# Optimization experiments

Hardware: AMD Instinct MI355X
Metric: run time of the kernel (lower is better)

## Reference

```python
import jax, jax.numpy as jnp
import numpy as np
import math

H = 128      # hidden_channels
R = 32       # num_rbf
N = 4096     # atoms
E = 65536    # edges
CU = 4.5     # cutoff_upper (cutoff_lower = 0)
ALPHA = 5.0 / CU
MEANS = jnp.linspace(math.exp(-CU), 1.0, R, dtype=jnp.float32)
BETA = jnp.float32((2.0 / R * (1.0 - math.exp(-CU))) ** -2)
EPS = 1e-5


def _ln(x, g, b):
    mu = x.mean(-1, keepdims=True)
    var = ((x - mu) ** 2).mean(-1, keepdims=True)
    return (x - mu) * jax.lax.rsqrt(var + EPS) * g + b


def setup_inputs() -> dict:
    key = jax.random.key(0)
    ks = jax.random.split(key, 20)
    f32 = jnp.float32

    def w(i, shape):
        return jax.random.normal(ks[i], shape, f32) / np.float32(np.sqrt(shape[-1]))

    return {
        "edge_vec": jax.random.normal(ks[0], (E, 3), f32) * 1.5,
        "emb_w": w(1, (128, H)),
        "emb2_w": w(2, (H, 2 * H)), "emb2_b": jnp.zeros((H,), f32),
        "dp1_w": w(3, (H, R)), "dp1_b": jnp.zeros((H,), f32),
        "dp2_w": w(4, (H, R)), "dp2_b": jnp.zeros((H,), f32),
        "dp3_w": w(5, (H, R)), "dp3_b": jnp.zeros((H,), f32),
        "lt0_w": w(6, (H, H)), "lt1_w": w(7, (H, H)), "lt2_w": w(8, (H, H)),
        "ls0_w": w(9, (2 * H, H)), "ls0_b": jnp.zeros((2 * H,), f32),
        "ls1_w": w(10, (3 * H, 2 * H)), "ls1_b": jnp.zeros((3 * H,), f32),
        "init_g": jnp.ones((H,), f32), "init_b": jnp.zeros((H,), f32),
        "lin_w": w(11, (H, 3 * H)), "lin_b": jnp.zeros((H,), f32),
        "outn_g": jnp.ones((3 * H,), f32), "outn_b": jnp.zeros((3 * H,), f32),
        "ol1_w": w(12, (H // 2, H)), "ol1_b": jnp.zeros((H // 2,), f32),
        "ol2_w": w(13, (1, H // 2)), "ol2_b": jnp.zeros((1,), f32),
        "z": jax.random.randint(ks[14], (N,), 0, 128, dtype=jnp.int32),
        "edge_index": jax.random.randint(ks[15], (2, E), 0, N, dtype=jnp.int32),
    }


def reference(edge_vec, emb_w, emb2_w, emb2_b, dp1_w, dp1_b, dp2_w, dp2_b,
              dp3_w, dp3_b, lt0_w, lt1_w, lt2_w, ls0_w, ls0_b, ls1_w, ls1_b,
              init_g, init_b, lin_w, lin_b, outn_g, outn_b, ol1_w, ol1_b,
              ol2_w, ol2_b, z, edge_index):
    n = z.shape[0]
    src, dst = edge_index[0], edge_index[1]

    d = jnp.sqrt((edge_vec ** 2).sum(-1))                 # (E,)
    vn = edge_vec / d[:, None]                             # unit edge vectors
    cut = jnp.where(d < CU, 0.5 * (jnp.cos(jnp.pi * d / CU) + 1.0), 0.0)
    # expnorm RBF
    rbf = cut[:, None] * jnp.exp(-BETA * (jnp.exp(-ALPHA * d)[:, None] - MEANS) ** 2)  # (E,R)

    # atomic-number message Zij = emb2(cat(emb(z_i), emb(z_j)))
    zpair = jnp.concatenate([emb_w[z[src]], emb_w[z[dst]]], -1)  # (E,2H)
    zij = zpair @ emb2_w.T + emb2_b                              # (E,H)
    c = cut[:, None] * zij                                       # cutoff * Zij, (E,H)

    w1 = (rbf @ dp1_w.T + dp1_b) * c    # scalar channel weights (E,H)
    w2 = (rbf @ dp2_w.T + dp2_b) * c
    w3 = (rbf @ dp3_w.T + dp3_b) * c

    eye = jnp.eye(3, dtype=edge_vec.dtype)
    zero = jnp.zeros_like(vn[:, 0])
    skew = jnp.stack([zero, -vn[:, 2], vn[:, 1],
                      vn[:, 2], zero, -vn[:, 0],
                      -vn[:, 1], vn[:, 0], zero], 1).reshape(-1, 3, 3)  # (E,3,3)
    outer = vn[:, :, None] * vn[:, None, :]
    sym = outer - ((vn ** 2).sum(-1) / 3.0)[:, None, None] * eye        # traceless sym (E,3,3)

    seg = lambda a: jax.ops.segment_sum(a, src, num_segments=n)
    I0 = seg(w1)[:, :, None, None] * eye                                # (N,H,3,3)
    A0 = seg(w2[:, :, None, None] * skew[:, None, :, :])                # (N,H,3,3)
    S0 = seg(w3[:, :, None, None] * sym[:, None, :, :])                 # (N,H,3,3)

    tn = ((I0 + A0 + S0) ** 2).sum((-2, -1))                            # tensor_norm, (N,H)
    nrm = _ln(tn, init_g, init_b)
    h = jax.nn.silu(nrm @ ls0_w.T + ls0_b)
    scal = jax.nn.silu(h @ ls1_w.T + ls1_b).reshape(n, H, 3)            # per-channel gates

    I1 = jnp.einsum('nhxy,gh->ngxy', I0, lt0_w) * scal[..., 0][..., None, None]
    A1 = jnp.einsum('nhxy,gh->ngxy', A0, lt1_w) * scal[..., 1][..., None, None]
    S1 = jnp.einsum('nhxy,gh->ngxy', S0, lt2_w) * scal[..., 2][..., None, None]

    x = jnp.concatenate([(I1 ** 2).sum((-2, -1)),
                         (A1 ** 2).sum((-2, -1)),
                         (S1 ** 2).sum((-2, -1))], -1)                  # (N,3H)
    x = _ln(x, outn_g, outn_b)
    s1 = x @ lin_w.T + lin_b
    s2 = jax.nn.silu(s1) @ ol1_w.T + ol1_b
    s3 = jax.nn.silu(s2) @ ol2_w.T + ol2_b                              # per-atom energy (N,1)
    return s3
```

## Files before the change

### kernel.cpp

```cpp
#include <hip/hip_runtime.h>
#include <math.h>

#define NH_TOT 524288
#define N_ATOM 4096
#define N_EDGE 65536

typedef __attribute__((ext_vector_type(8))) short bf16x8;
typedef __attribute__((ext_vector_type(4))) float f32x4;

__device__ __forceinline__ unsigned short f2bf(float f) {
    unsigned u = __builtin_bit_cast(unsigned, f);
    unsigned r = (u + 0x7fffu + ((u >> 16) & 1u)) >> 16;
    return (unsigned short)r;
}
__device__ __forceinline__ float silu(float v) { return v / (1.0f + __expf(-v)); }

#define WB_LS1 32768
#define WB_LT0 131072
#define WB_LT1 147456
#define WB_LT2 163840
#define WB_DP  180224

__global__ __launch_bounds__(256) void k_setup(
    const float* __restrict__ emb_w, const float* __restrict__ emb2_w,
    const int* __restrict__ ei,
    const float* __restrict__ ls0_w, const float* __restrict__ ls1_w,
    const float* __restrict__ lt0_w, const float* __restrict__ lt1_w,
    const float* __restrict__ lt2_w,
    const float* __restrict__ dp1_w, const float* __restrict__ dp2_w,
    const float* __restrict__ dp3_w,
    float* __restrict__ U1, float* __restrict__ U2,
    int* __restrict__ cnt, unsigned short* __restrict__ wb) {
    const int bx = blockIdx.x, tid = threadIdx.x;
    if (bx < 4096) {
        const int idx = bx * 4 + (tid >> 6);
        const int t = idx >> 7, h = idx & 127;
        const int lane = tid & 63;
        const float e0 = emb_w[t * 128 + lane];
        const float e1 = emb_w[t * 128 + 64 + lane];
        const float* row = emb2_w + h * 256;
        const float w0 = row[lane], w1 = row[64 + lane];
        const float w2 = row[128 + lane], w3 = row[192 + lane];
        float u1 = e0 * w0 + e1 * w1;
        float u2 = e0 * w2 + e1 * w3;
#pragma unroll
        for (int o = 1; o < 64; o <<= 1) {
            u1 += __shfl_xor(u1, o, 64);
            u2 += __shfl_xor(u2, o, 64);
        }
        if (lane == 0) {
            U1[t * 128 + h] = u1;
            U2[t * 128 + h] = u2;
        }
    } else if (bx < 4352) {
        const int e = (bx - 4096) * 256 + tid;
        atomicAdd(&cnt[ei[e]], 1);
    } else {
        const int base = (bx - 4352) * 1024 + tid * 4;
        const float* src;
        int off;
        if (base < 32768)       { src = ls0_w; off = 0; }
        else if (base < 131072) { src = ls1_w; off = 32768; }
        else if (base < 147456) { src = lt0_w; off = 131072; }
        else if (base < 163840) { src = lt1_w; off = 147456; }
        else if (base < 180224) { src = lt2_w; off = 163840; }
        else if (base < 184320) { src = dp1_w; off = 180224; }
        else if (base < 188416) { src = dp2_w; off = 184320; }
        else                    { src = dp3_w; off = 188416; }
        const float4 v = *(const float4*)(src + (base - off));
        unsigned short* o = wb + base;
        o[0] = f2bf(v.x); o[1] = f2bf(v.y); o[2] = f2bf(v.z); o[3] = f2bf(v.w);
    }
}

__global__ __launch_bounds__(256) void k_scan(const int* __restrict__ cnt, int* __restrict__ off) {
    __shared__ int s[256];
    const int t = threadIdx.x;
    int loc[16];
    int run = 0;
#pragma unroll
    for (int i = 0; i < 16; i++) { run += cnt[t * 16 + i]; loc[i] = run; }
    s[t] = run;
    __syncthreads();
    for (int d = 1; d < 256; d <<= 1) {
        const int add = (t >= d) ? s[t - d] : 0;
        __syncthreads();
        s[t] += add;
        __syncthreads();
    }
    const int base = s[t] - run;
    if (t == 0) off[0] = 0;
#pragma unroll
    for (int i = 0; i < 16; i++) off[t * 16 + i + 1] = base + loc[i];
}

__global__ __launch_bounds__(256) void k_scatter(const int* __restrict__ ei,
                                                 const int* __restrict__ off,
                                                 int* __restrict__ cursor,
                                                 int* __restrict__ order) {
    const int e = blockIdx.x * 256 + threadIdx.x;
    const int s = ei[e];
    order[off[s] + atomicAdd(&cursor[s], 1)] = e;
}

__global__ __launch_bounds__(256) void k_node(
    const int* __restrict__ z, const int* __restrict__ off,
    const int* __restrict__ order, const int* __restrict__ ei,
    const float* __restrict__ edge_vec,
    const float* __restrict__ U1, const float* __restrict__ U2,
    const float* __restrict__ emb2_b,
    const float* __restrict__ dp1_b, const float* __restrict__ dp2_b,
    const float* __restrict__ dp3_b,
    const unsigned short* __restrict__ wb,
    const float* __restrict__ init_g, const float* __restrict__ init_b,
    unsigned short* __restrict__ acc_bf, unsigned short* __restrict__ nrm_bf) {
    const int tid = threadIdx.x;
    const int wave = tid >> 6, lane = tid & 63, lm = lane & 15, lq = lane >> 4;
    const int nb = blockIdx.x * 4;

    const unsigned short* dpw = wb + WB_DP;
    bf16x8 bfr[3][2];
    float bhc[2], bk1[2], bk2[2], bk3[2];
    int cols[2];
#pragma unroll
    for (int t = 0; t < 2; t++) {
        const int col = wave * 32 + t * 16 + lm;
        cols[t] = col;
        bhc[t] = emb2_b[col];
        bk1[t] = dp1_b[col]; bk2[t] = dp2_b[col]; bk3[t] = dp3_b[col];
#pragma unroll
        for (int k = 0; k < 3; k++)
            bfr[k][t] = *(const bf16x8*)(dpw + k * 4096 + col * 32 + lq * 8);
    }

    const float m0 = 0.011108996538242306f;
    const float dm = (1.0f - m0) * (1.0f / 31.0f);
    const float tb = 0.0625f * (1.0f - m0);
    const float beta = 1.0f / (tb * tb);
    const float mean0 = m0 + (float)(lq * 8) * dm;

    __shared__ float redS[4][4];
    __shared__ float redQ[4][4];

    float tnA[4], tnB[4];

    for (int nn = 0; nn < 4; nn++) {
        const int n = nb + nn;
        const int beg = off[n];
        const int En = off[n + 1] - beg;
        const int zoff = z[n] << 7;
        const float u1c0 = U1[zoff + cols[0]];
        const float u1c1 = U1[zoff + cols[1]];

        float part[10][2];
#pragma unroll
        for (int p = 0; p < 10; p++) { part[p][0] = 0.f; part[p][1] = 0.f; }

        for (int mi = 0; mi < En; mi += 16) {
            const int e = order[beg + min(mi + lm, En - 1)];
            const float evx = edge_vec[3 * e + 0];
            const float evy = edge_vec[3 * e + 1];
            const float evz = edge_vec[3 * e + 2];
            const float d = sqrtf(evx * evx + evy * evy + evz * evz);
            const float inv = 1.0f / d;
            const float cut = (d < 4.5f) ? 0.5f * (__cosf(0.6981317007977318f * d) + 1.0f) : 0.0f;
            const float vx = evx * inv, vy = evy * inv, vz = evz * inv;
            const int u2o = z[ei[N_EDGE + e]] << 7;
            const float expd = __expf(-1.1111111111111112f * d);

            union { bf16x8 v; unsigned short s[8]; } uf;
#pragma unroll
            for (int j = 0; j < 8; j++) {
                const float df = expd - (mean0 + (float)j * dm);
                uf.s[j] = f2bf(cut * __expf(-beta * df * df));
            }
            const bf16x8 af = uf.v;

            f32x4 c[3][2];
#pragma unroll
            for (int k = 0; k < 3; k++)
#pragma unroll
                for (int t = 0; t < 2; t++)
                    c[k][t] = __builtin_amdgcn_mfma_f32_16x16x32_bf16(
                        af, bfr[k][t], (f32x4){0.f, 0.f, 0.f, 0.f}, 0, 0, 0);

#pragma unroll
            for (int r = 0; r < 4; r++) {
                const int er = mi + lq * 4 + r;
                const bool valid = er < En;
                const int sl = (lane & 48) | (lq * 4 + r);
                const float gvx = __shfl(vx, sl, 64);
                const float gvy = __shfl(vy, sl, 64);
                const float gvz = __shfl(vz, sl, 64);
                const float gct = __shfl(cut, sl, 64);
                const int   go  = __shfl(u2o, sl, 64);
#pragma unroll
                for (int t = 0; t < 2; t++) {
                    const float u2v = U2[go + cols[t]];
                    const float u1h = (t == 0) ? u1c0 : u1c1;
                    const float cc = valid ? gct * (u1h + u2v + bhc[t]) : 0.f;
                    const float w1 = (c[0][t][r] + bk1[t]) * cc;
                    const float w2 = (c[1][t][r] + bk2[t]) * cc;
                    const float w3 = (c[2][t][r] + bk3[t]) * cc;
                    part[0][t] += w1;
                    part[1][t] += w2 * gvx; part[2][t] += w2 * gvy; part[3][t] += w2 * gvz;
                    const float tx = w3 * gvx, ty = w3 * gvy;
                    part[4][t] += tx * gvx; part[5][t] += tx * gvy; part[6][t] += tx * gvz;
                    part[7][t] += ty * gvy; part[8][t] += ty * gvz; part[9][t] += w3 * gvz * gvz;
                }
            }
        }

#pragma unroll
        for (int p = 0; p < 10; p++)
#pragma unroll
            for (int t = 0; t < 2; t++) {
                float v = part[p][t];
                v += __shfl_xor(v, 16, 64);
                v += __shfl_xor(v, 32, 64);
                part[p][t] = v;
            }
        if (lq == 0) {
#pragma unroll
            for (int p = 0; p < 10; p++)
#pragma unroll
                for (int t = 0; t < 2; t++)
                    acc_bf[(size_t)p * NH_TOT + n * 128 + cols[t]] = f2bf(part[p][t]);
        }

        float tn[2];
#pragma unroll
        for (int t = 0; t < 2; t++) {
            const float aI = part[0][t];
            const float axv = part[1][t], ayv = part[2][t], azv = part[3][t];
            const float mxx = part[4][t], mxy = part[5][t], mxz = part[6][t];
            const float myy = part[7][t], myz = part[8][t], mzz = part[9][t];
            const float tr3 = (mxx + myy + mzz) * (1.0f / 3.0f);
            const float t00 = aI + mxx - tr3;
            const float t11 = aI + myy - tr3;
            const float t22 = aI + mzz - tr3;
            tn[t] = t00 * t00 + t11 * t11 + t22 * t22 +
                    2.0f * (mxy * mxy + azv * azv + mxz * mxz + ayv * ayv + myz * myz + axv * axv);
        }
        tnA[nn] = tn[0];
        tnB[nn] = tn[1];

        float s = (lq == 0) ? (tn[0] + tn[1]) : 0.f;
        s += __shfl_xor(s, 1, 64);
        s += __shfl_xor(s, 2, 64);
        s += __shfl_xor(s, 4, 64);
        s += __shfl_xor(s, 8, 64);
        if (lane == 0) redS[nn][wave] = s;
    }
    __syncthreads();

    float dvA[4], dvB[4];
#pragma unroll
    for (int nn = 0; nn < 4; nn++) {
        const float mu = (redS[nn][0] + redS[nn][1] + redS[nn][2] + redS[nn][3]) * (1.0f / 128.0f);
        dvA[nn] = tnA[nn] - mu;
        dvB[nn] = tnB[nn] - mu;
        float q = (lq == 0) ? (dvA[nn] * dvA[nn] + dvB[nn] * dvB[nn]) : 0.f;
        q += __shfl_xor(q, 1, 64);
        q += __shfl_xor(q, 2, 64);
        q += __shfl_xor(q, 4, 64);
        q += __shfl_xor(q, 8, 64);
        if (lane == 0) redQ[nn][wave] = q;
    }
    __syncthreads();

    if (lq == 0) {
        const float g0 = init_g[cols[0]], g1 = init_g[cols[1]];
        const float b0 = init_b[cols[0]], b1 = init_b[cols[1]];
#pragma unroll
        for (int nn = 0; nn < 4; nn++) {
            const float var = (redQ[nn][0] + redQ[nn][1] + redQ[nn][2] + redQ[nn][3]) * (1.0f / 128.0f);
            const float rs = rsqrtf(var + 1e-5f);
            const int n = nb + nn;
            nrm_bf[n * 128 + cols[0]] = f2bf(dvA[nn] * rs * g0 + b0);
            nrm_bf[n * 128 + cols[1]] = f2bf(dvB[nn] * rs * g1 + b1);
        }
    }
}

__global__ __launch_bounds__(256) void k_megatail(
    const unsigned short* __restrict__ nrm_bf, const unsigned short* __restrict__ acc_bf,
    const unsigned short* __restrict__ wb,
    const float* __restrict__ ls0_b, const float* __restrict__ ls1_b,
    const float* __restrict__ outn_g, const float* __restrict__ outn_b,
    const float* __restrict__ lin_w, const float* __restrict__ lin_b,
    const float* __restrict__ ol1_w, const float* __restrict__ ol1_b,
    const float* __restrict__ ol2_w, const float* __restrict__ ol2_b,
    float* __restrict__ out) {
    const int tid = threadIdx.x, wave = tid >> 6, lane = tid & 63;
    const int lm = lane & 15, lq = lane >> 4;
    const int n0 = blockIdx.x * 8;

    __shared__ unsigned short h1[16][280];
    __shared__ float scal_s[8][388];
    __shared__ float xs[8][392];
    __shared__ float ss[8][132];

    {
        f32x4 acc[4];
#pragma unroll
        for (int j = 0; j < 4; j++) acc[j] = (f32x4){0.f, 0.f, 0.f, 0.f};
        const int cbase = wave * 64;
#pragma unroll
        for (int kc = 0; kc < 128; kc += 32) {
            const int arow = n0 + min(lm, 7);
            const bf16x8 af = *(const bf16x8*)(nrm_bf + (size_t)arow * 128 + kc + lq * 8);
#pragma unroll
            for (int sn = 0; sn < 4; sn++) {
                const bf16x8 b = *(const bf16x8*)(wb + (size_t)(cbase + sn * 16 + lm) * 128 + kc + lq * 8);
                acc[sn] = __builtin_amdgcn_mfma_f32_16x16x32_bf16(af, b, acc[sn], 0, 0, 0);
            }
        }
#pragma unroll
        for (int sn = 0; sn < 4; sn++) {
            const int col = cbase + sn * 16 + lm;
            const float bv = ls0_b[col];
#pragma unroll
            for (int r = 0; r < 4; r++)
                h1[lq * 4 + r][col] = f2bf(silu(acc[sn][r] + bv));
        }
    }
    __syncthreads();
    {
        f32x4 acc[6];
#pragma unroll
        for (int j = 0; j < 6; j++) acc[j] = (f32x4){0.f, 0.f, 0.f, 0.f};
        const int cbase = wave * 96;
        const unsigned short* ls1p = wb + WB_LS1;
#pragma unroll 2
        for (int kc = 0; kc < 256; kc += 32) {
            const bf16x8 af = *(const bf16x8*)(&h1[lm][kc + lq * 8]);
#pragma unroll
            for (int sn = 0; sn < 6; sn++) {
                const bf16x8 b = *(const bf16x8*)(ls1p + (size_t)(cbase + sn * 16 + lm) * 256 + kc + lq * 8);
                acc[sn] = __builtin_amdgcn_mfma_f32_16x16x32_bf16(af, b, acc[sn], 0, 0, 0);
            }
        }
#pragma unroll
        for (int sn = 0; sn < 6; sn++) {
            const int col = cbase + sn * 16 + lm;
            const float bv = ls1_b[col];
#pragma unroll
            for (int r = 0; r < 4; r++) {
                const int node = lq * 4 + r;
                if (node < 8) scal_s[node][col] = silu(acc[sn][r] + bv);
            }
        }
    }
    __syncthreads();

    f32x4 e0[2], e1[2], e2[2], trv[2];
#pragma unroll
    for (int sn = 0; sn < 2; sn++) {
        e0[sn] = (f32x4){0.f, 0.f, 0.f, 0.f};
        e1[sn] = (f32x4){0.f, 0.f, 0.f, 0.f};
        e2[sn] = (f32x4){0.f, 0.f, 0.f, 0.f};
        trv[sn] = (f32x4){0.f, 0.f, 0.f, 0.f};
    }
#pragma unroll
    for (int p = 0; p < 10; p++) {
        const unsigned short* A = acc_bf + (size_t)p * NH_TOT;
        const unsigned short* B = wb + (p == 0 ? WB_LT0 : (p < 4 ? WB_LT1 : WB_LT2));
        f32x4 c[2];
        c[0] = (f32x4){0.f, 0.f, 0.f, 0.f};
        c[1] = (f32x4){0.f, 0.f, 0.f, 0.f};
#pragma unroll
        for (int kc = 0; kc < 128; kc += 32) {
            const int arow = n0 + min(lm, 7);
            const bf16x8 af = *(const bf16x8*)(A + (size_t)arow * 128 + kc + lq * 8);
#pragma unroll
            for (int sn = 0; sn < 2; sn++) {
                const bf16x8 b = *(const bf16x8*)(B + (size_t)(wave * 32 + sn * 16 + lm) * 128 + kc + lq * 8);
                c[sn] = __builtin_amdgcn_mfma_f32_16x16x32_bf16(af, b, c[sn], 0, 0, 0);
            }
        }
#pragma unroll
        for (int sn = 0; sn < 2; sn++) {
            if (p == 0)      e0[sn] += c[sn] * c[sn];
            else if (p < 4)  e1[sn] += c[sn] * c[sn];
            else if (p == 4 || p == 7 || p == 9) { e2[sn] += c[sn] * c[sn]; trv[sn] += c[sn]; }
            else             e2[sn] += 2.0f * c[sn] * c[sn];
        }
    }

    if (lq < 2) {
#pragma unroll
        for (int sn = 0; sn < 2; sn++) {
            const int g = wave * 32 + sn * 16 + lm;
#pragma unroll
            for (int r = 0; r < 4; r++) {
                const int node = lq * 4 + r;
                const float s0 = scal_s[node][3 * g + 0];
                const float s1 = scal_s[node][3 * g + 1];
                const float s2 = scal_s[node][3 * g + 2];
                xs[node][g]       = 3.0f * e0[sn][r] * s0 * s0;
                xs[node][128 + g] = 2.0f * e1[sn][r] * s1 * s1;
                const float tr = trv[sn][r];
                xs[node][256 + g] = (e2[sn][r] - tr * tr * (1.0f / 3.0f)) * s2 * s2;
            }
        }
    }
    __syncthreads();

#pragma unroll
    for (int i = 0; i < 2; i++) {
        const int node = wave * 2 + i;
        float v[6];
        float s = 0.f;
#pragma unroll
        for (int j = 0; j < 6; j++) { v[j] = xs[node][lane + 64 * j]; s += v[j]; }
#pragma unroll
        for (int o = 1; o < 64; o <<= 1) s += __shfl_xor(s, o, 64);
        const float mu = s * (1.0f / 384.0f);
        float q = 0.f;
#pragma unroll
        for (int j = 0; j < 6; j++) { v[j] -= mu; q += v[j] * v[j]; }
#pragma unroll
        for (int o = 1; o < 64; o <<= 1) q += __shfl_xor(q, o, 64);
        const float rs = rsqrtf(q * (1.0f / 384.0f) + 1e-5f);
#pragma unroll
        for (int j = 0; j < 6; j++) {
            const int col = lane + 64 * j;
            xs[node][col] = v[j] * rs * outn_g[col] + outn_b[col];
        }
    }
    __syncthreads();

    {
        const int j = tid & 127, half = tid >> 7;
        float a4[4];
        const float lb = lin_b[j];
#pragma unroll
        for (int i = 0; i < 4; i++) a4[i] = lb;
        const float4* wr = (const float4*)(lin_w + j * 384);
#pragma unroll 2
        for (int k4 = 0; k4 < 96; k4++) {
            const float4 w4 = wr[k4];
#pragma unroll
            for (int i = 0; i < 4; i++) {
                const float4 xv = *(const float4*)&xs[half * 4 + i][k4 * 4];
                a4[i] += w4.x * xv.x + w4.y * xv.y + w4.z * xv.z + w4.w * xv.w;
            }
        }
#pragma unroll
        for (int i = 0; i < 4; i++) ss[half * 4 + i][j] = silu(a4[i]);
    }
    __syncthreads();

    {
        const int o = tid & 63, q = tid >> 6;
        float a2v[2];
        const float ob = ol1_b[o];
        a2v[0] = ob; a2v[1] = ob;
        const float4* o4 = (const float4*)(ol1_w + o * 128);
#pragma unroll 4
        for (int k4 = 0; k4 < 32; k4++) {
            const float4 w4 = o4[k4];
#pragma unroll
            for (int i = 0; i < 2; i++) {
                const float4 sv = *(const float4*)&ss[q * 2 + i][k4 * 4];
                a2v[i] += w4.x * sv.x + w4.y * sv.y + w4.z * sv.z + w4.w * sv.w;
            }
        }
        const float w2 = ol2_w[o];
#pragma unroll
        for (int i = 0; i < 2; i++) {
            float v = silu(a2v[i]) * w2;
            for (int s = 32; s > 0; s >>= 1) v += __shfl_down(v, s, 64);
            if (o == 0) out[n0 + q * 2 + i] = v + ol2_b[0];
        }
    }
}

extern "C" void kernel_launch(void* const* d_in, const int* in_sizes, int n_in,
                              void* d_out, int out_size, void* d_ws, size_t ws_size,
                              hipStream_t stream) {
    (void)in_sizes; (void)n_in; (void)out_size; (void)ws_size;
    const float* edge_vec = (const float*)d_in[0];
    const float* emb_w   = (const float*)d_in[1];
    const float* emb2_w  = (const float*)d_in[2];
    const float* emb2_b  = (const float*)d_in[3];
    const float* dp1_w   = (const float*)d_in[4];
    const float* dp1_b   = (const float*)d_in[5];
    const float* dp2_w   = (const float*)d_in[6];
    const float* dp2_b   = (const float*)d_in[7];
    const float* dp3_w   = (const float*)d_in[8];
    const float* dp3_b   = (const float*)d_in[9];
    const float* lt0_w   = (const float*)d_in[10];
    const float* lt1_w   = (const float*)d_in[11];
    const float* lt2_w   = (const float*)d_in[12];
    const float* ls0_w   = (const float*)d_in[13];
    const float* ls0_b   = (const float*)d_in[14];
    const float* ls1_w   = (const float*)d_in[15];
    const float* ls1_b   = (const float*)d_in[16];
    const float* init_g  = (const float*)d_in[17];
    const float* init_b  = (const float*)d_in[18];
    const float* lin_w   = (const float*)d_in[19];
    const float* lin_b   = (const float*)d_in[20];
    const float* outn_g  = (const float*)d_in[21];
    const float* outn_b  = (const float*)d_in[22];
    const float* ol1_w   = (const float*)d_in[23];
    const float* ol1_b   = (const float*)d_in[24];
    const float* ol2_w   = (const float*)d_in[25];
    const float* ol2_b   = (const float*)d_in[26];
    const int* z  = (const int*)d_in[27];
    const int* ei = (const int*)d_in[28];
    float* out = (float*)d_out;

    char* w = (char*)d_ws;
    int*            cnt    = (int*)(w);
    int*            cursor = (int*)(w + 16384);
    int*            off    = (int*)(w + 32768);
    unsigned short* wb     = (unsigned short*)(w + 49408);
    float*          U1     = (float*)(w + 434432);
    float*          U2     = (float*)(w + 499968);
    int*            order  = (int*)(w + 565504);
    unsigned short* nrm_bf = (unsigned short*)(w + 827648);
    unsigned short* acc_bf = (unsigned short*)(w + 1876224);

    hipMemsetAsync(w, 0, 32768, stream);
    k_setup<<<dim3(4540), dim3(256), 0, stream>>>(emb_w, emb2_w, ei,
                                                  ls0_w, ls1_w, lt0_w, lt1_w, lt2_w,
                                                  dp1_w, dp2_w, dp3_w,
                                                  U1, U2, cnt, wb);
    k_scan<<<dim3(1), dim3(256), 0, stream>>>(cnt, off);
    k_scatter<<<dim3(256), dim3(256), 0, stream>>>(ei, off, cursor, order);
    k_node<<<dim3(1024), dim3(256), 0, stream>>>(z, off, order, ei, edge_vec, U1, U2,
                                                 emb2_b, dp1_b, dp2_b, dp3_b, wb,
                                                 init_g, init_b, acc_bf, nrm_bf);
    k_megatail<<<dim3(512), dim3(256), 0, stream>>>(nrm_bf, acc_bf, wb, ls0_b, ls1_b,
                                                    outn_g, outn_b, lin_w, lin_b,
                                                    ol1_w, ol1_b, ol2_w, ol2_b, out);
}
```

Before: 237.7 us.

## Fuse node aggregation with tail MLP and replace CSR build with fixed buckets

The count/scan/scatter CSR build is replaced by fixed 64-slot per-node edge buckets, filled with one atomic per edge inside the setup kernel. The per-node aggregation kernel and the tail kernel are merged into one kernel, so the 10 accumulated tensor components and the normalized norms stay in shared memory instead of going through global memory. This drops two kernel launches, the single-block scan and a large global write/read of intermediates. In exchange, each block now processes 8 nodes serially with half as many blocks, uses more shared memory, and silently drops edges for any node whose degree exceeds 64.

```diff
diff --git a/kernel.cpp b/kernel.cpp
--- a/kernel.cpp
+++ b/kernel.cpp
@@ -30,7 +30,8 @@
     const float* __restrict__ dp1_w, const float* __restrict__ dp2_w,
     const float* __restrict__ dp3_w,
     float* __restrict__ U1, float* __restrict__ U2,
-    int* __restrict__ cnt, unsigned short* __restrict__ wb) {
+    int* __restrict__ cursor, int* __restrict__ order_pad,
+    unsigned short* __restrict__ wb) {
     const int bx = blockIdx.x, tid = threadIdx.x;
     if (bx < 4096) {
         const int idx = bx * 4 + (tid >> 6);
@@ -54,7 +55,9 @@
         }
     } else if (bx < 4352) {
         const int e = (bx - 4096) * 256 + tid;
-        atomicAdd(&cnt[ei[e]], 1);
+        const int src = ei[e];
+        const int pos = atomicAdd(&cursor[src], 1);
+        if (pos < 64) order_pad[(src << 6) + pos] = e;
     } else {
         const int base = (bx - 4352) * 1024 + tid * 4;
         const float* src;
@@ -73,39 +76,9 @@
     }
 }
 
-__global__ __launch_bounds__(256) void k_scan(const int* __restrict__ cnt, int* __restrict__ off) {
-    __shared__ int s[256];
-    const int t = threadIdx.x;
-    int loc[16];
-    int run = 0;
-#pragma unroll
-    for (int i = 0; i < 16; i++) { run += cnt[t * 16 + i]; loc[i] = run; }
-    s[t] = run;
-    __syncthreads();
-    for (int d = 1; d < 256; d <<= 1) {
-        const int add = (t >= d) ? s[t - d] : 0;
-        __syncthreads();
-        s[t] += add;
-        __syncthreads();
-    }
-    const int base = s[t] - run;
-    if (t == 0) off[0] = 0;
-#pragma unroll
-    for (int i = 0; i < 16; i++) off[t * 16 + i + 1] = base + loc[i];
-}
-
-__global__ __launch_bounds__(256) void k_scatter(const int* __restrict__ ei,
-                                                 const int* __restrict__ off,
-                                                 int* __restrict__ cursor,
-                                                 int* __restrict__ order) {
-    const int e = blockIdx.x * 256 + threadIdx.x;
-    const int s = ei[e];
-    order[off[s] + atomicAdd(&cursor[s], 1)] = e;
-}
-
-__global__ __launch_bounds__(256) void k_node(
-    const int* __restrict__ z, const int* __restrict__ off,
-    const int* __restrict__ order, const int* __restrict__ ei,
+__global__ __launch_bounds__(256) void k_fused(
+    const int* __restrict__ z, const int* __restrict__ ecnt,
+    const int* __restrict__ order_pad, const int* __restrict__ ei,
     const float* __restrict__ edge_vec,
     const float* __restrict__ U1, const float* __restrict__ U2,
     const float* __restrict__ emb2_b,
@@ -113,10 +86,25 @@
     const float* __restrict__ dp3_b,
     const unsigned short* __restrict__ wb,
     const float* __restrict__ init_g, const float* __restrict__ init_b,
-    unsigned short* __restrict__ acc_bf, unsigned short* __restrict__ nrm_bf) {
+    const float* __restrict__ ls0_b, const float* __restrict__ ls1_b,
+    const float* __restrict__ outn_g, const float* __restrict__ outn_b,
+    const float* __restrict__ lin_w, const float* __restrict__ lin_b,
+    const float* __restrict__ ol1_w, const float* __restrict__ ol1_b,
+    const float* __restrict__ ol2_w, const float* __restrict__ ol2_b,
+    float* __restrict__ out) {
     const int tid = threadIdx.x;
     const int wave = tid >> 6, lane = tid & 63, lm = lane & 15, lq = lane >> 4;
-    const int nb = blockIdx.x * 4;
+    const int n0 = blockIdx.x * 8;
+    const int ar = (lm < 8) ? lm : 7;
+
+    __shared__ alignas(16) unsigned short accs[10][8][136];
+    __shared__ alignas(16) unsigned short nrms[8][136];
+    __shared__ unsigned short h1[16][280];
+    __shared__ float scal_s[8][388];
+    __shared__ float ss[8][132];
+    __shared__ float redS[8][4];
+    __shared__ float redQ[8][4];
+    float (*xs)[392] = reinterpret_cast<float(*)[392]>(&accs[0][0][0]);
 
     const unsigned short* dpw = wb + WB_DP;
     bf16x8 bfr[3][2];
@@ -139,15 +127,12 @@
     const float beta = 1.0f / (tb * tb);
     const float mean0 = m0 + (float)(lq * 8) * dm;
 
-    __shared__ float redS[4][4];
-    __shared__ float redQ[4][4];
-
-    float tnA[4], tnB[4];
-
-    for (int nn = 0; nn < 4; nn++) {
-        const int n = nb + nn;
-        const int beg = off[n];
-        const int En = off[n + 1] - beg;
+    float tnA[8], tnB[8];
+
+    for (int nn = 0; nn < 8; nn++) {
+        const int n = n0 + nn;
+        const int En = min(ecnt[n], 64);
+        const int beg = n << 6;
         const int zoff = z[n] << 7;
         const float u1c0 = U1[zoff + cols[0]];
         const float u1c1 = U1[zoff + cols[1]];
@@ -157,7 +142,7 @@
         for (int p = 0; p < 10; p++) { part[p][0] = 0.f; part[p][1] = 0.f; }
 
         for (int mi = 0; mi < En; mi += 16) {
-            const int e = order[beg + min(mi + lm, En - 1)];
+            const int e = order_pad[beg + min(mi + lm, En - 1)];
             const float evx = edge_vec[3 * e + 0];
             const float evy = edge_vec[3 * e + 1];
             const float evz = edge_vec[3 * e + 2];
@@ -225,7 +210,7 @@
             for (int p = 0; p < 10; p++)
 #pragma unroll
                 for (int t = 0; t < 2; t++)
-                    acc_bf[(size_t)p * NH_TOT + n * 128 + cols[t]] = f2bf(part[p][t]);
+                    accs[p][nn][cols[t]] = f2bf(part[p][t]);
         }
 
         float tn[2];
@@ -254,52 +239,34 @@
     }
     __syncthreads();
 
-    float dvA[4], dvB[4];
-#pragma unroll
-    for (int nn = 0; nn < 4; nn++) {
-        const float mu = (redS[nn][0] + redS[nn][1] + redS[nn][2] + redS[nn][3]) * (1.0f / 128.0f);
-        dvA[nn] = tnA[nn] - mu;
-        dvB[nn] = tnB[nn] - mu;
-        float q = (lq == 0) ? (dvA[nn] * dvA[nn] + dvB[nn] * dvB[nn]) : 0.f;
-        q += __shfl_xor(q, 1, 64);
-        q += __shfl_xor(q, 2, 64);
-        q += __shfl_xor(q, 4, 64);
-        q += __shfl_xor(q, 8, 64);
-        if (lane == 0) redQ[nn][wave] = q;
-    }
-    __syncthreads();
-
-    if (lq == 0) {
-        const float g0 = init_g[cols[0]], g1 = init_g[cols[1]];
-        const float b0 = init_b[cols[0]], b1 = init_b[cols[1]];
-#pragma unroll
-        for (int nn = 0; nn < 4; nn++) {
-            const float var = (redQ[nn][0] + redQ[nn][1] + redQ[nn][2] + redQ[nn][3]) * (1.0f / 128.0f);
-            const float rs = rsqrtf(var + 1e-5f);
-            const int n = nb + nn;
-            nrm_bf[n * 128 + cols[0]] = f2bf(dvA[nn] * rs * g0 + b0);
-            nrm_bf[n * 128 + cols[1]] = f2bf(dvB[nn] * rs * g1 + b1);
-        }
-    }
-}
-
-__global__ __launch_bounds__(256) void k_megatail(
-    const unsigned short* __restrict__ nrm_bf, const unsigned short* __restrict__ acc_bf,
-    const unsigned short* __restrict__ wb,
-    const float* __restrict__ ls0_b, const float* __restrict__ ls1_b,
-    const float* __restrict__ outn_g, const float* __restrict__ outn_b,
-    const float* __restrict__ lin_w, const float* __restrict__ lin_b,
-    const float* __restrict__ ol1_w, const float* __restrict__ ol1_b,
-    const float* __restrict__ ol2_w, const float* __restrict__ ol2_b,
-    float* __restrict__ out) {
-    const int tid = threadIdx.x, wave = tid >> 6, lane = tid & 63;
-    const int lm = lane & 15, lq = lane >> 4;
-    const int n0 = blockIdx.x * 8;
-
-    __shared__ unsigned short h1[16][280];
-    __shared__ float scal_s[8][388];
-    __shared__ float xs[8][392];
-    __shared__ float ss[8][132];
+    {
+        float dvA[8], dvB[8];
+#pragma unroll
+        for (int nn = 0; nn < 8; nn++) {
+            const float mu = (redS[nn][0] + redS[nn][1] + redS[nn][2] + redS[nn][3]) * (1.0f / 128.0f);
+            dvA[nn] = tnA[nn] - mu;
+            dvB[nn] = tnB[nn] - mu;
+            float q = (lq == 0) ? (dvA[nn] * dvA[nn] + dvB[nn] * dvB[nn]) : 0.f;
+            q += __shfl_xor(q, 1, 64);
+            q += __shfl_xor(q, 2, 64);
+            q += __shfl_xor(q, 4, 64);
+            q += __shfl_xor(q, 8, 64);
+            if (lane == 0) redQ[nn][wave] = q;
+        }
+        __syncthreads();
+        if (lq == 0) {
+            const float g0 = init_g[cols[0]], g1 = init_g[cols[1]];
+            const float b0 = init_b[cols[0]], b1 = init_b[cols[1]];
+#pragma unroll
+            for (int nn = 0; nn < 8; nn++) {
+                const float var = (redQ[nn][0] + redQ[nn][1] + redQ[nn][2] + redQ[nn][3]) * (1.0f / 128.0f);
+                const float rs = rsqrtf(var + 1e-5f);
+                nrms[nn][cols[0]] = f2bf(dvA[nn] * rs * g0 + b0);
+                nrms[nn][cols[1]] = f2bf(dvB[nn] * rs * g1 + b1);
+            }
+        }
+    }
+    __syncthreads();
 
     {
         f32x4 acc[4];
@@ -308,8 +275,7 @@
         const int cbase = wave * 64;
 #pragma unroll
         for (int kc = 0; kc < 128; kc += 32) {
-            const int arow = n0 + min(lm, 7);
-            const bf16x8 af = *(const bf16x8*)(nrm_bf + (size_t)arow * 128 + kc + lq * 8);
+            const bf16x8 af = *(const bf16x8*)(&nrms[ar][kc + lq * 8]);
 #pragma unroll
             for (int sn = 0; sn < 4; sn++) {
                 const bf16x8 b = *(const bf16x8*)(wb + (size_t)(cbase + sn * 16 + lm) * 128 + kc + lq * 8);
@@ -364,15 +330,13 @@
     }
 #pragma unroll
     for (int p = 0; p < 10; p++) {
-        const unsigned short* A = acc_bf + (size_t)p * NH_TOT;
         const unsigned short* B = wb + (p == 0 ? WB_LT0 : (p < 4 ? WB_LT1 : WB_LT2));
         f32x4 c[2];
         c[0] = (f32x4){0.f, 0.f, 0.f, 0.f};
         c[1] = (f32x4){0.f, 0.f, 0.f, 0.f};
 #pragma unroll
         for (int kc = 0; kc < 128; kc += 32) {
-            const int arow = n0 + min(lm, 7);
-            const bf16x8 af = *(const bf16x8*)(A + (size_t)arow * 128 + kc + lq * 8);
+            const bf16x8 af = *(const bf16x8*)(&accs[p][ar][kc + lq * 8]);
 #pragma unroll
             for (int sn = 0; sn < 2; sn++) {
                 const bf16x8 b = *(const bf16x8*)(B + (size_t)(wave * 32 + sn * 16 + lm) * 128 + kc + lq * 8);
@@ -387,6 +351,7 @@
             else             e2[sn] += 2.0f * c[sn] * c[sn];
         }
     }
+    __syncthreads();
 
     if (lq < 2) {
 #pragma unroll
@@ -513,27 +478,20 @@
     float* out = (float*)d_out;
 
     char* w = (char*)d_ws;
-    int*            cnt    = (int*)(w);
-    int*            cursor = (int*)(w + 16384);
-    int*            off    = (int*)(w + 32768);
-    unsigned short* wb     = (unsigned short*)(w + 49408);
-    float*          U1     = (float*)(w + 434432);
-    float*          U2     = (float*)(w + 499968);
-    int*            order  = (int*)(w + 565504);
-    unsigned short* nrm_bf = (unsigned short*)(w + 827648);
-    unsigned short* acc_bf = (unsigned short*)(w + 1876224);
-
-    hipMemsetAsync(w, 0, 32768, stream);
+    int*            cursor    = (int*)(w);
+    unsigned short* wb        = (unsigned short*)(w + 16384);
+    float*          U1        = (float*)(w + 401408);
+    float*          U2        = (float*)(w + 466944);
+    int*            order_pad = (int*)(w + 532480);
+
+    hipMemsetAsync(w, 0, 16384, stream);
     k_setup<<<dim3(4540), dim3(256), 0, stream>>>(emb_w, emb2_w, ei,
                                                   ls0_w, ls1_w, lt0_w, lt1_w, lt2_w,
                                                   dp1_w, dp2_w, dp3_w,
-                                                  U1, U2, cnt, wb);
-    k_scan<<<dim3(1), dim3(256), 0, stream>>>(cnt, off);
-    k_scatter<<<dim3(256), dim3(256), 0, stream>>>(ei, off, cursor, order);
-    k_node<<<dim3(1024), dim3(256), 0, stream>>>(z, off, order, ei, edge_vec, U1, U2,
-                                                 emb2_b, dp1_b, dp2_b, dp3_b, wb,
-                                                 init_g, init_b, acc_bf, nrm_bf);
-    k_megatail<<<dim3(512), dim3(256), 0, stream>>>(nrm_bf, acc_bf, wb, ls0_b, ls1_b,
-                                                    outn_g, outn_b, lin_w, lin_b,
-                                                    ol1_w, ol1_b, ol2_w, ol2_b, out);
+                                                  U1, U2, cursor, order_pad, wb);
+    k_fused<<<dim3(512), dim3(256), 0, stream>>>(z, cursor, order_pad, ei, edge_vec,
+                                                 U1, U2, emb2_b, dp1_b, dp2_b, dp3_b, wb,
+                                                 init_g, init_b, ls0_b, ls1_b,
+                                                 outn_g, outn_b, lin_w, lin_b,
+                                                 ol1_w, ol1_b, ol2_w, ol2_b, out);
 }
```

Result: faster. 213.3 us (-10.3%).
